# Performance work log

Measured on AMD Instinct MI355X. Metric: run time of the kernel, lower is better.

Reference implementation:

```python
import jax, jax.numpy as jnp
import numpy as np

B, N, D = 256, 512, 512
H = 512            # step_context_dim
HEADS = 8
KEY = H // HEADS
T = 128            # number of decode steps
TANH_CLIP = 10.0
TEMP = 1.0
VEHICLE_CAP = 1.0
BATTERY_CAP = 1.0
NEG = -1e9         # stands in for -inf; safe under softmax/vjp


def setup_inputs() -> dict:
    key = jax.random.key(0)
    ks = jax.random.split(key, 10)
    embedding = jax.random.normal(ks[0], (B, N, D), dtype=jnp.float32)
    current_nodes = jax.random.randint(ks[1], (B, T), 0, N)
    used_capacity = jax.random.uniform(ks[2], (B, T), dtype=jnp.float32)
    used_battery = jax.random.uniform(ks[3], (B, T), dtype=jnp.float32)
    current_time = jax.random.uniform(ks[4], (B, T), dtype=jnp.float32)
    mask = jax.random.randint(ks[5], (B, T, N), 0, 2).astype(bool)
    mask = mask.at[:, :, 0].set(False)  # ensure at least one feasible node
    s = 0.02
    W_context = jax.random.normal(ks[6], (D, H), dtype=jnp.float32) * s
    W_kvlogit = jax.random.normal(ks[7], (D, 3 * H), dtype=jnp.float32) * s
    W_step = jax.random.normal(ks[8], (D + 3, H), dtype=jnp.float32) * s
    W_out = jax.random.normal(ks[9], (H, H), dtype=jnp.float32) * s
    return {"embedding": embedding, "current_nodes": current_nodes,
            "used_capacity": used_capacity, "used_battery": used_battery,
            "current_time": current_time, "mask": mask,
            "W_context": W_context, "W_kvlogit": W_kvlogit,
            "W_step": W_step, "W_out": W_out}


def reference(embedding, current_nodes, used_capacity, used_battery,
              current_time, mask, W_context, W_kvlogit, W_step, W_out):
    b, n, d = embedding.shape
    t = current_nodes.shape[1]
    # fixed context from mean graph embedding: [B,1,H]
    fixed_context = jnp.einsum('bd,dh->bh', embedding.mean(axis=1), W_context)[:, None, :]
    # shared K/V/logit-K projections: [B,N,3H]
    kvl = jnp.einsum('bnd,de->bne', embedding, W_kvlogit)
    glimpse_K, glimpse_V, logit_K = jnp.split(kvl, 3, axis=-1)
    glimpse_K = glimpse_K.reshape(b, n, HEADS, KEY).transpose(0, 2, 1, 3)  # [B,h,N,k]
    glimpse_V = glimpse_V.reshape(b, n, HEADS, KEY).transpose(0, 2, 1, 3)  # [B,h,N,k]
    # per-step context: gathered current-node embedding + 3 scalar state features
    cur_emb = jnp.take_along_axis(
        embedding, current_nodes[:, :, None], axis=1)  # [B,T,D]
    next_nodes = jnp.concatenate(
        [cur_emb,
         (VEHICLE_CAP - used_capacity)[..., None],
         (BATTERY_CAP - used_battery)[..., None],
         current_time[..., None]], axis=-1)            # [B,T,D+3]
    query = fixed_context + jnp.einsum('btd,dh->bth', next_nodes, W_step)  # [B,T,H]
    # multi-head single-query glimpse attention over all T steps at once
    Q = query.reshape(b, t, HEADS, KEY)
    compat = jnp.einsum('bthk,bhnk->bhtn', Q, glimpse_K) / np.sqrt(KEY)
    compat = jnp.where(mask[:, None, :, :], NEG, compat)
    attn = jax.nn.softmax(compat, axis=-1)
    heads_out = jnp.einsum('bhtn,bhnk->bthk', attn, glimpse_V).reshape(b, t, H)
    glimpse = jnp.einsum('bth,ho->bto', heads_out, W_out)  # project_out
    logits = jnp.einsum('bth,bnh->btn', glimpse, logit_K) / np.sqrt(H)
    logits = jnp.tanh(logits) * TANH_CLIP
    logits = jnp.where(mask, NEG, logits)
    log_p = jax.nn.log_softmax(logits / TEMP, axis=-1)  # [B,T,N]
    return log_p
```

## Files before the change

kernel.cpp:

```cpp
#include <hip/hip_runtime.h>
#include <hip/hip_bf16.h>
#include <hip/hip_fp8.h>
#include <stdint.h>

typedef unsigned char  u8;
typedef unsigned short u16;
typedef unsigned int   u32;
typedef unsigned long long u64;
typedef __attribute__((ext_vector_type(4))) float f32x4;
typedef __attribute__((ext_vector_type(8))) short s16x8;

#define NEG_INF (-1e9f)

__device__ __forceinline__ u16 f2bf(float f) {
  __hip_bfloat16 h = __float2bfloat16(f);
  return __builtin_bit_cast(u16, h);
}

__device__ __forceinline__ u8 f2fp8(float f) {
  __hip_fp8_e4m3 h(f);
  return (u8)h.__x;
}

#if defined(__has_builtin)
#if __has_builtin(__builtin_amdgcn_cvt_pk_fp8_f32)
#define HAVE_PK8 1
#endif
#endif

__device__ __forceinline__ u32 pk4_fp8(float a, float b, float c, float d) {
#ifdef HAVE_PK8
  int r = __builtin_amdgcn_cvt_pk_fp8_f32(a, b, 0, false);
  r = __builtin_amdgcn_cvt_pk_fp8_f32(c, d, r, true);
  return (u32)r;
#else
  return (u32)f2fp8(a) | ((u32)f2fp8(b) << 8) | ((u32)f2fp8(c) << 16) |
         ((u32)f2fp8(d) << 24);
#endif
}

__device__ __forceinline__ f32x4 mfma16(s16x8 a, s16x8 b, f32x4 c) {
  return __builtin_amdgcn_mfma_f32_16x16x32_bf16(a, b, c, 0, 0, 0);
}

__device__ __forceinline__ f32x4 mfma8(long a, long b, f32x4 c) {
  return __builtin_amdgcn_mfma_f32_16x16x32_fp8_fp8(a, b, c, 0, 0, 0);
}

#define GLOAD16(g, l)                                                        \
  __builtin_amdgcn_global_load_lds(                                          \
      (const __attribute__((address_space(1))) unsigned int*)(g),            \
      (__attribute__((address_space(3))) unsigned int*)(l), 16, 0, 0)
#define GLOAD4(g, l)                                                         \
  __builtin_amdgcn_global_load_lds(                                          \
      (const __attribute__((address_space(1))) unsigned int*)(g),            \
      (__attribute__((address_space(3))) unsigned int*)(l), 4, 0, 0)

#define WAITV(n) asm volatile("s_waitcnt vmcnt(" #n ")" ::: "memory")
#define WAITLGKM asm volatile("s_waitcnt lgkmcnt(0)" ::: "memory")
#define SBAR __builtin_amdgcn_sched_barrier(0)
#define HBAR __builtin_amdgcn_s_barrier()

__global__ void detect_mask_kernel(const u32* __restrict__ mraw, u32* __restrict__ flag) {
  __shared__ int any;
  if (threadIdx.x == 0) any = 0;
  __syncthreads();
  int loc = 0;
  for (int i = threadIdx.x; i < 16384; i += 256) {
    u32 v = mraw[i];
    if (v & 0xFFFFFF00u) loc = 1;
  }
  if (loc) atomicOr(&any, 1);
  __syncthreads();
  if (threadIdx.x == 0) *flag = any ? 1u : 4u;
}

__global__ __launch_bounds__(256) void maskprep_kernel(const void* __restrict__ mraw,
                                                       const u32* __restrict__ flag,
                                                       unsigned char* __restrict__ mb) {
  long long idx = (long long)blockIdx.x * 256 + threadIdx.x;
  long long bt = idx >> 6;
  int ch = (int)(idx & 63);
  unsigned char byte = 0;
  if (*flag == 1) {
    u64 v = *(const u64*)((const unsigned char*)mraw + bt * 512 + ch * 8);
#pragma unroll
    for (int i = 0; i < 8; i++)
      if ((v >> (8 * i)) & 0xFFull) byte |= (unsigned char)(1 << i);
  } else {
    const int* p = (const int*)mraw + bt * 512 + ch * 8;
#pragma unroll
    for (int i = 0; i < 8; i++)
      if (p[i]) byte |= (unsigned char)(1 << i);
  }
  mb[idx] = byte;
}

__global__ void tcvt8_kernel(const float* __restrict__ in, int ld_in, int kreal,
                             int CO, u8* __restrict__ outp) {
  int i = blockIdx.x;
  for (int j = threadIdx.x; j < CO; j += 256) {
    float v = (j < kreal) ? in[(long long)j * ld_in + i] * 16.0f : 0.0f;
    outp[(long long)i * CO + j] = f2fp8(v);
  }
}

__global__ void slice_cvt_kernel(const float* __restrict__ in, u16* __restrict__ outp) {
  long long idx = (long long)blockIdx.x * 256 + threadIdx.x;
  long long dd = idx >> 9;
  int hh = (int)(idx & 511);
  outp[idx] = f2bf(in[dd * 1536 + 1024 + hh]);
}

__global__ void cvt_bf_kernel(const float* __restrict__ in, u16* __restrict__ outp) {
  long long idx = (long long)blockIdx.x * 256 + threadIdx.x;
  outp[idx] = f2bf(in[idx]);
}

__global__ __launch_bounds__(256) void cvt_pmean_kernel(const float* __restrict__ emb,
                                                        u8* __restrict__ e8,
                                                        float* __restrict__ pmean) {
  const int bq = blockIdx.x >> 2, nq = blockIdx.x & 3;
  const int tid = threadIdx.x;
  const int ro = tid >> 7;
  const int c4 = (tid & 127) << 2;
  const long long base = ((long long)bq * 512 + nq * 128) * 512;
  float s[4] = {0.f, 0.f, 0.f, 0.f};
  for (int n = ro; n < 128; n += 2) {
    f32x4 v = *(const f32x4*)&emb[base + (long long)n * 512 + c4];
#pragma unroll
    for (int i = 0; i < 4; i++) s[i] += v[i];
    *(u32*)&e8[base + (long long)n * 512 + c4] = pk4_fp8(v[0], v[1], v[2], v[3]);
  }
  __shared__ float ls[2][512];
#pragma unroll
  for (int i = 0; i < 4; i++) ls[ro][c4 + i] = s[i];
  __syncthreads();
  float* dst = pmean + (long long)blockIdx.x * 512;
  dst[tid] = ls[0][tid] + ls[1][tid];
  dst[tid + 256] = ls[0][tid + 256] + ls[1][tid + 256];
}

__global__ __launch_bounds__(256) void fixedctx_kernel(const float* __restrict__ pmean,
                                                       const float* __restrict__ Wc,
                                                       float* __restrict__ fixedc) {
  __shared__ float mf[512];
  int b = blockIdx.x;
  const float* p = pmean + (long long)b * 4 * 512;
  for (int d = threadIdx.x; d < 512; d += 256)
    mf[d] = (p[d] + p[512 + d] + p[1024 + d] + p[1536 + d]) * (1.0f / 512.0f);
  __syncthreads();
  for (int h = threadIdx.x; h < 512; h += 256) {
    float s = 0.f;
    for (int d = 0; d < 512; ++d) s += mf[d] * Wc[(long long)d * 512 + h];
    fixedc[(long long)b * 512 + h] = s;
  }
}

__global__ __launch_bounds__(256) void build_nextn8_kernel(
    const u8* __restrict__ e8, const int* __restrict__ cur,
    const float* __restrict__ ucap, const float* __restrict__ ubat,
    const float* __restrict__ ctim, u8* __restrict__ outp) {
  const long long rowm = (long long)blockIdx.x * 4 + (threadIdx.x >> 6);
  const int lane = threadIdx.x & 63;
  const int b = (int)(rowm >> 7);
  const int node = cur[rowm];
  const u8* src = e8 + ((long long)b * 512 + node) * 512;
  u8* dst = outp + rowm * 576;
  *(u64*)&dst[lane * 8] = *(const u64*)&src[lane * 8];
  if (lane < 8) {
    u64 v = 0;
    if (lane == 0) {
      v = (u64)f2fp8(1.0f - ucap[rowm]) | ((u64)f2fp8(1.0f - ubat[rowm]) << 8) |
          ((u64)f2fp8(ctim[rowm]) << 16);
    }
    *(u64*)&dst[512 + lane * 8] = v;
  }
}

__global__ __launch_bounds__(512, 4) void gemm_kv8_kernel(
    const u8* __restrict__ A8, const u8* __restrict__ Bw8,
    u8* __restrict__ K8, u8* __restrict__ V8) {
  __shared__ __align__(16) char lds[49152];
  const int tid = threadIdx.x;
  const int lane = tid & 63;
  const int wid = tid >> 6;
  const int wr = wid >> 1, wc = wid & 1;
  const int fr = lane & 15;
  const int fq = lane >> 4;

  const int p = blockIdx.x;
  const int x = p & 7;
  const int i = p >> 3;
  const int ntile = i & 7;
  const int mgrp = i >> 3;
  const long long nrow0 = (long long)ntile * 128;

  const int srow = tid >> 2;
  const int sc = tid & 3;

#define MROW(tt2) (((long long)x * 64 + mgrp * 8 + ((tt2) >> 3)) * 256)
#define KOF(tt2) (((tt2) & 7) * 64)

#define STAGEA(dd, tt2)                                                       \
  {                                                                           \
    _Pragma("unroll") for (int g_ = 0; g_ < 2; g_++) {                        \
      const int r_ = g_ * 128 + srow;                                         \
      GLOAD16(A8 + (MROW(tt2) + r_) * 512ll + KOF(tt2) +                      \
                  ((sc ^ ((r_ >> 1) & 3)) << 4),                              \
              lds + (dd) * 24576 + g_ * 8192 + wid * 1024);                   \
    }                                                                         \
  }
#define STAGEB(dd, tt2)                                                       \
  {                                                                           \
    GLOAD16(Bw8 + (nrow0 + srow) * 512ll + KOF(tt2) +                         \
                ((sc ^ ((srow >> 1) & 3)) << 4),                              \
            lds + (dd) * 24576 + 16384 + wid * 1024);                         \
  }

#define READ_A(dst, mb)                                                       \
  _Pragma("unroll") for (int ks = 0; ks < 2; ks++) {                          \
    const int r_ = wr * 64 + (mb) * 16 + fr;                                  \
    dst[ks] = *(const long*)(ab + r_ * 64 + (((ks * 4 + fq) ^ (r_ & 6)) << 3)); \
  }
#define MFMA_PH(src, mb)                                                      \
  _Pragma("unroll") for (int nb = 0; nb < 4; nb++)                            \
  _Pragma("unroll") for (int ks = 0; ks < 2; ks++)                            \
    acc[mb][nb] = mfma8(src[ks], bfrag[nb][ks], acc[mb][nb]);

  STAGEB(0, 0); STAGEA(0, 0);
  STAGEB(1, 1); STAGEA(1, 1);

  f32x4 acc[4][4];

#pragma unroll 1
  for (int u = 0; u < 8; u++) {
#pragma unroll
    for (int ii = 0; ii < 4; ii++)
#pragma unroll
      for (int jj = 0; jj < 4; jj++) acc[ii][jj] = (f32x4){0.f, 0.f, 0.f, 0.f};

#pragma unroll 1
    for (int t8 = 0; t8 < 8; t8++) {
      const int tt = u * 8 + t8;
      const int d = tt & 1;
      if (tt == 63) { WAITV(0); } else { WAITV(3); }
      HBAR; SBAR;

      const char* ab = lds + d * 24576;
      const char* bb = lds + d * 24576 + 16384;

      long bfrag[4][2];
#pragma unroll
      for (int nb = 0; nb < 4; nb++)
#pragma unroll
        for (int ks = 0; ks < 2; ks++) {
          const int brow = wc * 64 + nb * 16 + fr;
          bfrag[nb][ks] =
              *(const long*)(bb + brow * 64 + (((ks * 4 + fq) ^ (brow & 6)) << 3));
        }
      long afA[2], afB[2];
      READ_A(afA, 0);
      WAITLGKM; SBAR;
      READ_A(afB, 1);
      __builtin_amdgcn_s_setprio(1);
      MFMA_PH(afA, 0);
      __builtin_amdgcn_s_setprio(0);
      WAITLGKM; SBAR;
      READ_A(afA, 2);
      __builtin_amdgcn_s_setprio(1);
      MFMA_PH(afB, 1);
      __builtin_amdgcn_s_setprio(0);
      WAITLGKM; SBAR;
      READ_A(afB, 3);
      __builtin_amdgcn_s_setprio(1);
      MFMA_PH(afA, 2);
      __builtin_amdgcn_s_setprio(0);
      WAITLGKM; SBAR;
      HBAR;
      if (tt + 2 < 64) { STAGEB(d, tt + 2); STAGEA(d, tt + 2); }
      __builtin_amdgcn_s_setprio(1);
      MFMA_PH(afB, 3);
      __builtin_amdgcn_s_setprio(0);
    }

    const long long mrow0 = MROW(u * 8);
    const int colbase = (int)(ntile * 128) + wc * 64;
#pragma unroll
    for (int mb = 0; mb < 4; mb++) {
      const long long row = mrow0 + wr * 64 + mb * 16 + fq * 4;
      const int bbx = (int)(row >> 9);
      const int node0 = (int)(row & 511);
#pragma unroll
      for (int nb = 0; nb < 4; nb++) {
        const int col = colbase + nb * 16 + fr;
        const int hh = (col >> 6) & 7;
        const int kk = col & 63;
        const u32 pw = pk4_fp8(acc[mb][nb][0] * 0.0625f, acc[mb][nb][1] * 0.0625f,
                               acc[mb][nb][2] * 0.0625f, acc[mb][nb][3] * 0.0625f);
        if (col < 512) {
          u8* dst = K8 + (((long long)(bbx * 8 + hh) * 512 + node0) << 6) + kk;
#pragma unroll
          for (int q = 0; q < 4; q++)
            dst[(long long)q << 6] = (u8)(pw >> (8 * q));
        } else {
          *(u32*)(V8 + (((long long)(bbx * 8 + hh) * 64 + kk) << 9) + node0) = pw;
        }
      }
    }
  }
#undef STAGEA
#undef STAGEB
#undef READ_A
#undef MFMA_PH
#undef MROW
#undef KOF
}

template <int MODE>
__global__ __launch_bounds__(512, 4) void gemm8_kernel(
    const u8* __restrict__ A8, const u8* __restrict__ B8,
    int ldA, int ldB, int NT,
    u8* __restrict__ out0, const float* __restrict__ aux) {
  __shared__ __align__(16) char lds[49152];
  const int tid = threadIdx.x;
  const int lane = tid & 63;
  const int wid = tid >> 6;
  const int wr = wid >> 1, wc = wid & 1;
  const int fr = lane & 15;
  const int fq = lane >> 4;

  const int p = blockIdx.x;
  const int wk = (p & 7) * 64 + (p >> 3);
  const int mtile = wk >> 2;
  const int ntile = wk & 3;
  const long long mrow0 = (long long)mtile * 256;
  const long long nrow0 = (long long)ntile * 128;

  const int srow = tid >> 2;
  const int sc = tid & 3;

#define STAGEA8(dd, k0)                                                       \
  {                                                                           \
    _Pragma("unroll") for (int g_ = 0; g_ < 2; g_++) {                        \
      const int r_ = g_ * 128 + srow;                                         \
      GLOAD16(A8 + (mrow0 + r_) * (long long)ldA + (k0) +                     \
                  ((sc ^ ((r_ >> 1) & 3)) << 4),                              \
              lds + (dd) * 24576 + g_ * 8192 + wid * 1024);                   \
    }                                                                         \
  }
#define STAGEB8(dd, k0)                                                       \
  {                                                                           \
    GLOAD16(B8 + (nrow0 + srow) * (long long)ldB + (k0) +                     \
                ((sc ^ ((srow >> 1) & 3)) << 4),                              \
            lds + (dd) * 24576 + 16384 + wid * 1024);                         \
  }
#define READ_A8(dst, mb)                                                      \
  _Pragma("unroll") for (int ks = 0; ks < 2; ks++) {                          \
    const int r_ = wr * 64 + (mb) * 16 + fr;                                  \
    dst[ks] = *(const long*)(ab + r_ * 64 + (((ks * 4 + fq) ^ (r_ & 6)) << 3)); \
  }
#define MFMA_PH8(src, mb)                                                     \
  _Pragma("unroll") for (int nb = 0; nb < 4; nb++)                            \
  _Pragma("unroll") for (int ks = 0; ks < 2; ks++)                            \
    acc[mb][nb] = mfma8(src[ks], bfrag[nb][ks], acc[mb][nb]);

  f32x4 acc[4][4];
#pragma unroll
  for (int ii = 0; ii < 4; ii++)
#pragma unroll
    for (int jj = 0; jj < 4; jj++) acc[ii][jj] = (f32x4){0.f, 0.f, 0.f, 0.f};

  STAGEB8(0, 0); STAGEA8(0, 0);
  STAGEB8(1, 64); STAGEA8(1, 64);

#pragma unroll 1
  for (int t = 0; t < NT; t++) {
    const int d = t & 1;
    if (t == NT - 1) { WAITV(0); } else { WAITV(3); }
    HBAR; SBAR;

    const char* ab = lds + d * 24576;
    const char* bb = lds + d * 24576 + 16384;

    long bfrag[4][2];
#pragma unroll
    for (int nb = 0; nb < 4; nb++)
#pragma unroll
      for (int ks = 0; ks < 2; ks++) {
        const int brow = wc * 64 + nb * 16 + fr;
        bfrag[nb][ks] =
            *(const long*)(bb + brow * 64 + (((ks * 4 + fq) ^ (brow & 6)) << 3));
      }
    long afA[2], afB[2];
    READ_A8(afA, 0);
    WAITLGKM; SBAR;
    READ_A8(afB, 1);
    __builtin_amdgcn_s_setprio(1);
    MFMA_PH8(afA, 0);
    __builtin_amdgcn_s_setprio(0);
    WAITLGKM; SBAR;
    READ_A8(afA, 2);
    __builtin_amdgcn_s_setprio(1);
    MFMA_PH8(afB, 1);
    __builtin_amdgcn_s_setprio(0);
    WAITLGKM; SBAR;
    READ_A8(afB, 3);
    __builtin_amdgcn_s_setprio(1);
    MFMA_PH8(afA, 2);
    __builtin_amdgcn_s_setprio(0);
    WAITLGKM; SBAR;
    HBAR;
    if (t + 2 < NT) { STAGEB8(d, (t + 2) * 64); STAGEA8(d, (t + 2) * 64); }
    __builtin_amdgcn_s_setprio(1);
    MFMA_PH8(afB, 3);
    __builtin_amdgcn_s_setprio(0);
  }
#undef STAGEA8
#undef STAGEB8
#undef READ_A8
#undef MFMA_PH8

  const int colbase = (int)(ntile * 128) + wc * 64;
#pragma unroll
  for (int mb = 0; mb < 4; mb++) {
    const long long row0 = mrow0 + wr * 64 + mb * 16 + fq * 4;
#pragma unroll
    for (int nb = 0; nb < 4; nb++) {
      const int col = colbase + nb * 16 + fr;
      u32 pw;
      if (MODE == 0) {
        float v0 = acc[mb][nb][0] * 0.0625f + aux[((row0 + 0) >> 7) * 512 + col];
        float v1 = acc[mb][nb][1] * 0.0625f + aux[((row0 + 1) >> 7) * 512 + col];
        float v2 = acc[mb][nb][2] * 0.0625f + aux[((row0 + 2) >> 7) * 512 + col];
        float v3 = acc[mb][nb][3] * 0.0625f + aux[((row0 + 3) >> 7) * 512 + col];
        pw = pk4_fp8(v0 * 2.0f, v1 * 2.0f, v2 * 2.0f, v3 * 2.0f);
      } else {
        pw = pk4_fp8(acc[mb][nb][0] * 0.03125f, acc[mb][nb][1] * 0.03125f,
                     acc[mb][nb][2] * 0.03125f, acc[mb][nb][3] * 0.03125f);
      }
#pragma unroll
      for (int q = 0; q < 4; q++)
        out0[(row0 + q) * 512 + col] = (u8)(pw >> (8 * q));
    }
  }
}

__global__ __launch_bounds__(512, 4) void gemm_lsm8_kernel(
    const u8* __restrict__ e8, const u8* __restrict__ tmp8,
    const u64* __restrict__ maskb, float* __restrict__ outp) {
  __shared__ __align__(16) char lds[73728];
  const int tid = threadIdx.x;
  const int lane = tid & 63;
  const int wid = tid >> 6;
  const int fr = lane & 15;
  const int fq = lane >> 4;

  const int p = blockIdx.x;
  const int x = p & 7;
  const int i = p >> 3;
  const int thalf = i & 1;
  const int b = x * 32 + (i >> 1);

  const u8* Ab = e8 + (long long)b * 262144;
  const u8* Bb = tmp8 + (long long)b * 65536 + (long long)thalf * 64 * 512;

  const int srow = tid >> 2;
  const int sc = tid & 3;

#define STAGEA(dd, k0)                                                        \
  {                                                                           \
    _Pragma("unroll") for (int g_ = 0; g_ < 4; g_++) {                        \
      const int r_ = g_ * 128 + srow;                                         \
      GLOAD16(Ab + r_ * 512ll + (k0) + ((sc ^ ((r_ >> 1) & 3)) << 4),         \
              lds + (dd) * 32768 + g_ * 8192 + wid * 1024);                   \
    }                                                                         \
  }
#define STAGEB(dd, k0)                                                        \
  {                                                                           \
    _Pragma("unroll") for (int g_ = 0; g_ < 2; g_++) {                        \
      const int r_ = g_ * 32 + (tid >> 4);                                    \
      const int lb_ = (tid & 15) * 4;                                         \
      const int gb_ = ((((lb_ >> 4) ^ ((r_ >> 1) & 3))) << 4) | (lb_ & 15);   \
      GLOAD4(Bb + r_ * 512ll + (k0) + gb_,                                    \
             lds + 65536 + (dd) * 4096 + g_ * 2048 + wid * 256);              \
    }                                                                         \
  }
#define READ_A(dst, mb)                                                       \
  _Pragma("unroll") for (int ks = 0; ks < 2; ks++) {                          \
    const int r_ = wid * 64 + (mb) * 16 + fr;                                 \
    dst[ks] = *(const long*)(ab + r_ * 64 + (((ks * 4 + fq) ^ (r_ & 6)) << 3)); \
  }
#define MFMA_PH(src, mb)                                                      \
  _Pragma("unroll") for (int nb = 0; nb < 4; nb++)                            \
  _Pragma("unroll") for (int ks = 0; ks < 2; ks++)                            \
    acc[mb][nb] = mfma8(src[ks], bfrag[nb][ks], acc[mb][nb]);

  f32x4 acc[4][4];
#pragma unroll
  for (int ii = 0; ii < 4; ii++)
#pragma unroll
    for (int jj = 0; jj < 4; jj++) acc[ii][jj] = (f32x4){0.f, 0.f, 0.f, 0.f};

  STAGEB(0, 0); STAGEA(0, 0);
  STAGEB(1, 64); STAGEA(1, 64);

#pragma unroll 1
  for (int t = 0; t < 8; t++) {
    const int d = t & 1;
    if (t == 7) { WAITV(0); } else { WAITV(6); }
    HBAR; SBAR;

    const char* ab = lds + d * 32768;
    const char* bb = lds + 65536 + d * 4096;

    long bfrag[4][2];
#pragma unroll
    for (int nb = 0; nb < 4; nb++)
#pragma unroll
      for (int ks = 0; ks < 2; ks++) {
        const int brow = nb * 16 + fr;
        bfrag[nb][ks] =
            *(const long*)(bb + brow * 64 + (((ks * 4 + fq) ^ (brow & 6)) << 3));
      }
    long afA[2], afB[2];
    READ_A(afA, 0);
    WAITLGKM; SBAR;
    READ_A(afB, 1);
    __builtin_amdgcn_s_setprio(1);
    MFMA_PH(afA, 0);
    __builtin_amdgcn_s_setprio(0);
    WAITLGKM; SBAR;
    READ_A(afA, 2);
    __builtin_amdgcn_s_setprio(1);
    MFMA_PH(afB, 1);
    __builtin_amdgcn_s_setprio(0);
    WAITLGKM; SBAR;
    READ_A(afB, 3);
    __builtin_amdgcn_s_setprio(1);
    MFMA_PH(afA, 2);
    __builtin_amdgcn_s_setprio(0);
    WAITLGKM; SBAR;
    HBAR;
    if (t + 2 < 8) { STAGEB(d, (t + 2) * 64); STAGEA(d, (t + 2) * 64); }
    __builtin_amdgcn_s_setprio(1);
    MFMA_PH(afB, 3);
    __builtin_amdgcn_s_setprio(0);
  }
#undef STAGEA
#undef STAGEB
#undef READ_A
#undef MFMA_PH

  float* red = (float*)lds;
  const float rs8 = 0.044194173824159216f * 0.125f;
  const float L2E = 1.4426950408889634f;

  float lmax[4];
#pragma unroll
  for (int nb = 0; nb < 4; nb++) {
    const int tl = nb * 16 + fr;
    const long long orow = (long long)b * 128 + thalf * 64 + tl;
    const u64 w = maskb[orow * 8 + wid];
    float mx = -3.0e38f;
#pragma unroll
    for (int mb = 0; mb < 4; mb++) {
      f32x4 r;
#pragma unroll
      for (int q = 0; q < 4; q++) {
        float xv = acc[mb][nb][q] * rs8;
        float e = exp2f(xv * 2.8853900817779268f);
        float th = 1.0f - 2.0f * __builtin_amdgcn_rcpf(e + 1.0f);
        float lg = 10.0f * th;
        const int bitn = mb * 16 + fq * 4 + q;
        if ((w >> bitn) & 1ull) lg = NEG_INF;
        r[q] = lg;
        mx = fmaxf(mx, lg);
      }
      acc[mb][nb] = r;
    }
    mx = fmaxf(mx, __shfl_xor(mx, 16));
    mx = fmaxf(mx, __shfl_xor(mx, 32));
    lmax[nb] = mx;
  }
  __syncthreads();
  if (lane < 16) {
#pragma unroll
    for (int nb = 0; nb < 4; nb++) red[wid * 64 + nb * 16 + lane] = lmax[nb];
  }
  __syncthreads();
  if (tid < 64) {
    float m = red[tid];
#pragma unroll
    for (int ww = 1; ww < 8; ww++) m = fmaxf(m, red[ww * 64 + tid]);
    red[512 + tid] = m;
  }
  __syncthreads();
  float lsum[4];
#pragma unroll
  for (int nb = 0; nb < 4; nb++) {
    const float m = red[512 + nb * 16 + fr];
    float s = 0.f;
#pragma unroll
    for (int mb = 0; mb < 4; mb++)
#pragma unroll
      for (int q = 0; q < 4; q++) s += exp2f((acc[mb][nb][q] - m) * L2E);
    s += __shfl_xor(s, 16);
    s += __shfl_xor(s, 32);
    lsum[nb] = s;
  }
  if (lane < 16) {
#pragma unroll
    for (int nb = 0; nb < 4; nb++) red[576 + wid * 64 + nb * 16 + lane] = lsum[nb];
  }
  __syncthreads();
  if (tid < 64) {
    float s = red[576 + tid];
#pragma unroll
    for (int ww = 1; ww < 8; ww++) s += red[576 + ww * 64 + tid];
    red[1088 + tid] = red[512 + tid] + logf(s);
  }
  __syncthreads();
#pragma unroll
  for (int nb = 0; nb < 4; nb++) {
    const int tl = nb * 16 + fr;
    const long long orow = (long long)b * 128 + thalf * 64 + tl;
    const float lse = red[1088 + tl];
#pragma unroll
    for (int mb = 0; mb < 4; mb++) {
      const int node0 = wid * 64 + mb * 16 + fq * 4;
      f32x4 r = acc[mb][nb];
#pragma unroll
      for (int q = 0; q < 4; q++) r[q] -= lse;
      *(f32x4*)&outp[orow * 512 + node0] = r;
    }
  }
}

__global__ __launch_bounds__(256) void gemm128_plain_kernel(
    const u16* __restrict__ A, const u16* __restrict__ Bv, u8* __restrict__ outp) {
  __shared__ u16 lA[128 * 32];
  __shared__ u16 lB[128 * 32];
  const int tid = threadIdx.x;
  const int lane = tid & 63;
  const int wave = tid >> 6;
  const int wr = wave >> 1, wc = wave & 1;

  const int p = blockIdx.x;
  const int wk = (p & 7) * 2 + (p >> 3);
  const int ntile = wk & 3;
  const int mtile = wk >> 2;
  const long long arow0 = (long long)mtile * 128;
  const long long brow0 = (long long)ntile * 128;

  f32x4 acc[4][4];
#pragma unroll
  for (int i = 0; i < 4; i++)
#pragma unroll
    for (int j = 0; j < 4; j++) acc[i][j] = (f32x4){0.f, 0.f, 0.f, 0.f};

  const int sc8 = (lane & 3) << 3;

  for (int k0 = 0; k0 < 512; k0 += 32) {
    __syncthreads();
#pragma unroll
    for (int i = 0; i < 2; i++) {
      GLOAD16(A + (arow0 + i * 64 + wave * 16 + (lane >> 2)) * 512ll + k0 + sc8,
              &lA[(i * 64 + wave * 16) * 32]);
      GLOAD16(Bv + (brow0 + i * 64 + wave * 16 + (lane >> 2)) * 512ll + k0 + sc8,
              &lB[(i * 64 + wave * 16) * 32]);
    }
    __syncthreads();
    s16x8 af[4], bfr[4];
#pragma unroll
    for (int i = 0; i < 4; i++)
      af[i] = *(const s16x8*)&lA[(wr * 64 + i * 16 + (lane & 15)) * 32 + ((lane >> 4) << 3)];
#pragma unroll
    for (int j = 0; j < 4; j++)
      bfr[j] = *(const s16x8*)&lB[(wc * 64 + j * 16 + (lane & 15)) * 32 + ((lane >> 4) << 3)];
#pragma unroll
    for (int i = 0; i < 4; i++)
#pragma unroll
      for (int j = 0; j < 4; j++) acc[i][j] = mfma16(af[i], bfr[j], acc[i][j]);
  }

#pragma unroll
  for (int i = 0; i < 4; i++) {
    const int rl = wr * 64 + i * 16 + ((lane >> 4) << 2);
#pragma unroll
    for (int j = 0; j < 4; j++) {
      const int cl = wc * 64 + j * 16 + (lane & 15);
#pragma unroll
      for (int q = 0; q < 4; q++)
        outp[(arow0 + rl + q) * 512 + brow0 + cl] = f2fp8(acc[i][j][q] * 64.0f);
    }
  }
}

__global__ __launch_bounds__(512, 4) void attn_kernel(
    const u8* __restrict__ q8, const u8* __restrict__ K8,
    const u8* __restrict__ V8, const u64* __restrict__ maskbits,
    u8* __restrict__ o8buf) {
  __shared__ __align__(16) char lds[68864];
  char* Plds = lds + 32768;
  float* rsw = (float*)(lds + 66560);
  float* rst = (float*)(lds + 68608);

  const int p = blockIdx.x;
  const int fb = (p & 7) * 512 + (p >> 3);
  const int thalf = fb & 1;
  const int h = (fb >> 1) & 7;
  const int b = fb >> 4;
  const int bh = b * 8 + h;
  const int tid = threadIdx.x;
  const int lane = tid & 63;
  const int wid = tid >> 6;
  const int fr = lane & 15;
  const int fq = lane >> 4;
  const int tt0 = thalf * 64;

  {
    const u8* Vb = V8 + (long long)bh * 32768;
#pragma unroll
    for (int it = 0; it < 4; it++) {
      const int row = it * 16 + (tid >> 5);
      const int s16 = tid & 31;
      GLOAD16(Vb + row * 512 + ((s16 ^ (row & 7)) << 4), lds + row * 512);
    }
  }

  const u8* Qb = q8 + ((long long)(b * 128 + tt0)) * 512 + h * 64;
  long qf[4][2];
#pragma unroll
  for (int tf = 0; tf < 4; tf++)
#pragma unroll
    for (int ks = 0; ks < 2; ks++)
      qf[tf][ks] = *(const long*)(Qb + (long long)(tf * 16 + fr) * 512 + ks * 32 + fq * 8);

  const int wstrip = wid * 64;
  const u8* Kb = K8 + ((long long)bh * 512 + wstrip) * 64;
  f32x4 s[4][4];
#pragma unroll
  for (int nf = 0; nf < 4; nf++)
#pragma unroll
    for (int tf = 0; tf < 4; tf++) s[nf][tf] = (f32x4){0.f, 0.f, 0.f, 0.f};
#pragma unroll
  for (int nf = 0; nf < 4; nf++) {
#pragma unroll
    for (int ks = 0; ks < 2; ks++) {
      long kf = *(const long*)(Kb + (long long)(nf * 16 + fr) * 64 + ks * 32 + fq * 8);
#pragma unroll
      for (int tf = 0; tf < 4; tf++) s[nf][tf] = mfma8(kf, qf[tf][ks], s[nf][tf]);
    }
  }

  const float CE2 = 0.09016844005556021f;
  u64 mq[4];
#pragma unroll
  for (int tf = 0; tf < 4; tf++)
    mq[tf] = maskbits[((long long)(b * 128) + tt0 + tf * 16 + fr) * 8 + wid];
  float psum[4] = {0.f, 0.f, 0.f, 0.f};
#pragma unroll
  for (int nf = 0; nf < 4; nf++) {
#pragma unroll
    for (int tf = 0; tf < 4; tf++) {
      float pv[4];
#pragma unroll
      for (int q = 0; q < 4; q++) {
        const int bit = nf * 16 + fq * 4 + q;
        float v = exp2f(s[nf][tf][q] * CE2);
        if ((mq[tf] >> bit) & 1ull) v = 0.0f;
        psum[tf] += v;
        pv[q] = v;
      }
      const u32 pw = pk4_fp8(pv[0], pv[1], pv[2], pv[3]);
      const int t = tf * 16 + fr;
      const int o = wstrip + nf * 16 + fq * 4;
      const int s8 = o >> 3, lo = o & 7;
      *(u32*)(Plds + t * 528 + (((s8 ^ (t & 7)) << 3) | lo)) = pw;
    }
  }
#pragma unroll
  for (int tf = 0; tf < 4; tf++) {
    float v = psum[tf];
    v += __shfl_xor(v, 16);
    v += __shfl_xor(v, 32);
    if (lane < 16) rsw[(tf * 16 + lane) * 8 + wid] = v;
  }
  __syncthreads();

  if (tid < 64) {
    float sum = rsw[tid * 8];
#pragma unroll
    for (int ww = 1; ww < 8; ww++) sum += rsw[tid * 8 + ww];
    rst[tid] = __builtin_amdgcn_rcpf(sum);
  }

  const int kkh = wid & 1;
  const int tts = wid >> 1;
  f32x4 o[2];
  o[0] = (f32x4){0.f, 0.f, 0.f, 0.f};
  o[1] = (f32x4){0.f, 0.f, 0.f, 0.f};
  const int tpv = tts * 16 + fr;
#pragma unroll
  for (int nstep = 0; nstep < 16; nstep++) {
    const int s8 = nstep * 4 + fq;
    long pf = *(const long*)(Plds + tpv * 528 + ((s8 ^ (tpv & 7)) << 3));
#pragma unroll
    for (int kf = 0; kf < 2; kf++) {
      const int kk = kkh * 32 + kf * 16 + fr;
      const int vs16 = s8 >> 1, vlo = s8 & 1;
      long vf = *(const long*)(lds + kk * 512 + (((vs16 ^ (kk & 7)) << 4) | (vlo << 3)));
      o[kf] = mfma8(vf, pf, o[kf]);
    }
  }
  __syncthreads();

  const float r4 = rst[tpv] * 4.0f;
  const long long orow = (long long)b * 128 + tt0 + tpv;
#pragma unroll
  for (int kf = 0; kf < 2; kf++) {
    const u32 pw = pk4_fp8(o[kf][0] * r4, o[kf][1] * r4, o[kf][2] * r4, o[kf][3] * r4);
    const int col = h * 64 + kkh * 32 + kf * 16 + fq * 4;
    *(u32*)&o8buf[orow * 512 + col] = pw;
  }
}

extern "C" void kernel_launch(void* const* d_in, const int* in_sizes, int n_in,
                              void* d_out, int out_size, void* d_ws, size_t ws_size,
                              hipStream_t stream) {
  (void)in_sizes; (void)n_in; (void)out_size; (void)ws_size;
  const float* emb  = (const float*)d_in[0];
  const int*   cur  = (const int*)d_in[1];
  const float* ucap = (const float*)d_in[2];
  const float* ubat = (const float*)d_in[3];
  const float* ctim = (const float*)d_in[4];
  const void*  mask = d_in[5];
  const float* Wc   = (const float*)d_in[6];
  const float* Wkvl = (const float*)d_in[7];
  const float* Wstep= (const float*)d_in[8];
  const float* Wout = (const float*)d_in[9];

  char* w = (char*)d_ws;
  size_t off = 0;
  auto take = [&](size_t nbytes) -> char* {
    char* p = w + off;
    off += (nbytes + 255) & ~(size_t)255;
    return p;
  };
  u32* flag            = (u32*)take(4);
  unsigned char* maskb = (unsigned char*)take((size_t)256 * 128 * 64);
  u8* e8               = (u8*)take((size_t)256 * 512 * 512);
  u8* WkT8             = (u8*)take((size_t)1024 * 512);
  u8* WstepT8          = (u8*)take((size_t)512 * 576);
  u16* W2bf            = (u16*)take((size_t)512 * 512 * 2);
  u16* Woutbf          = (u16*)take((size_t)512 * 512 * 2);
  u8* WfT8             = (u8*)take((size_t)512 * 512);
  float* pmean         = (float*)take((size_t)1024 * 512 * 4);
  float* fixedc        = (float*)take((size_t)256 * 512 * 4);
  u8* K8               = (u8*)take((size_t)256 * 8 * 512 * 64);
  u8* V8               = (u8*)take((size_t)256 * 8 * 64 * 512);
  u8* nextn8           = (u8*)take((size_t)32768 * 576);
  u8* q8               = (u8*)take((size_t)32768 * 512);
  u8* o8               = (u8*)take((size_t)32768 * 512);
  u8* tmp8             = (u8*)take((size_t)32768 * 512);

  detect_mask_kernel<<<1, 256, 0, stream>>>((const u32*)mask, flag);
  maskprep_kernel<<<8192, 256, 0, stream>>>(mask, flag, maskb);
  tcvt8_kernel<<<1024, 256, 0, stream>>>(Wkvl, 1536, 512, 512, WkT8);
  tcvt8_kernel<<<512, 256, 0, stream>>>(Wstep, 512, 515, 576, WstepT8);
  slice_cvt_kernel<<<1024, 256, 0, stream>>>(Wkvl, W2bf);
  cvt_bf_kernel<<<1024, 256, 0, stream>>>(Wout, Woutbf);
  gemm128_plain_kernel<<<16, 256, 0, stream>>>(W2bf, Woutbf, WfT8);
  cvt_pmean_kernel<<<1024, 256, 0, stream>>>(emb, e8, pmean);
  fixedctx_kernel<<<256, 256, 0, stream>>>(pmean, Wc, fixedc);
  build_nextn8_kernel<<<8192, 256, 0, stream>>>(e8, cur, ucap, ubat, ctim, nextn8);

  gemm_kv8_kernel<<<512, 512, 0, stream>>>(e8, WkT8, K8, V8);
  gemm8_kernel<0><<<512, 512, 0, stream>>>(nextn8, WstepT8, 576, 576, 9, q8, fixedc);
  attn_kernel<<<4096, 512, 0, stream>>>(q8, K8, V8, (const u64*)maskb, o8);
  gemm8_kernel<1><<<512, 512, 0, stream>>>(o8, WfT8, 512, 512, 8, tmp8, nullptr);
  gemm_lsm8_kernel<<<512, 512, 0, stream>>>(e8, tmp8, (const u64*)maskb, (float*)d_out);
}
```

Before: 501.3 us.

## Stage K/V epilogue through LDS for coalesced 16-byte stores and retile V layout

```diff
diff --git a/kernel.cpp b/kernel.cpp
--- a/kernel.cpp
+++ b/kernel.cpp
@@ -8,6 +8,7 @@
 typedef unsigned int   u32;
 typedef unsigned long long u64;
 typedef __attribute__((ext_vector_type(4))) float f32x4;
+typedef __attribute__((ext_vector_type(4))) unsigned int u32x4;
 typedef __attribute__((ext_vector_type(8))) short s16x8;
 
 #define NEG_INF (-1e9f)
@@ -181,7 +182,7 @@
 __global__ __launch_bounds__(512, 4) void gemm_kv8_kernel(
     const u8* __restrict__ A8, const u8* __restrict__ Bw8,
     u8* __restrict__ K8, u8* __restrict__ V8) {
-  __shared__ __align__(16) char lds[49152];
+  __shared__ __align__(16) char lds[57344];
   const int tid = threadIdx.x;
   const int lane = tid & 63;
   const int wid = tid >> 6;
@@ -232,6 +233,8 @@
   STAGEB(1, 1); STAGEA(1, 1);
 
   f32x4 acc[4][4];
+  char* tile = lds + 49152 + wid * 1024;
+  const int hh = (ntile * 2 + wc) & 7;
 
 #pragma unroll 1
   for (int u = 0; u < 8; u++) {
@@ -285,27 +288,52 @@
     }
 
     const long long mrow0 = MROW(u * 8);
-    const int colbase = (int)(ntile * 128) + wc * 64;
-#pragma unroll
-    for (int mb = 0; mb < 4; mb++) {
-      const long long row = mrow0 + wr * 64 + mb * 16 + fq * 4;
-      const int bbx = (int)(row >> 9);
-      const int node0 = (int)(row & 511);
-#pragma unroll
-      for (int nb = 0; nb < 4; nb++) {
-        const int col = colbase + nb * 16 + fr;
-        const int hh = (col >> 6) & 7;
-        const int kk = col & 63;
-        const u32 pw = pk4_fp8(acc[mb][nb][0] * 0.0625f, acc[mb][nb][1] * 0.0625f,
-                               acc[mb][nb][2] * 0.0625f, acc[mb][nb][3] * 0.0625f);
-        if (col < 512) {
-          u8* dst = K8 + (((long long)(bbx * 8 + hh) * 512 + node0) << 6) + kk;
-#pragma unroll
-          for (int q = 0; q < 4; q++)
-            dst[(long long)q << 6] = (u8)(pw >> (8 * q));
-        } else {
-          *(u32*)(V8 + (((long long)(bbx * 8 + hh) * 64 + kk) << 9) + node0) = pw;
+    const int bbx = (int)(mrow0 >> 9);
+    const int nodeb = (int)(mrow0 & 511);
+    const long long bhoff = ((long long)(bbx * 8 + hh)) << 15;
+
+    if (ntile < 4) {
+#pragma unroll
+      for (int mb = 0; mb < 4; mb++) {
+#pragma unroll
+        for (int nb = 0; nb < 4; nb++) {
+          const u32 pw = pk4_fp8(acc[mb][nb][0] * 0.0625f, acc[mb][nb][1] * 0.0625f,
+                                 acc[mb][nb][2] * 0.0625f, acc[mb][nb][3] * 0.0625f);
+          const int colhi = (nb * 16 + (fr & ~3));
+          const int collo = fr & 3;
+#pragma unroll
+          for (int q = 0; q < 4; q++) {
+            const int row = fq * 4 + q;
+            tile[row * 64 + (colhi ^ ((row & 15) << 2)) + collo] = (u8)(pw >> (8 * q));
+          }
         }
+        WAITLGKM; SBAR;
+        const int row = lane >> 2;
+        u32x4 val;
+#pragma unroll
+        for (int j = 0; j < 4; j++) {
+          const int dw = ((lane & 3) * 4 + j) << 2;
+          val[j] = *(const u32*)(tile + row * 64 + (dw ^ ((row & 15) << 2)));
+        }
+        WAITLGKM; SBAR;
+        u8* dst = K8 + bhoff + (long long)(nodeb + wr * 64 + mb * 16) * 64;
+        *(u32x4*)(dst + lane * 16) = val;
+      }
+    } else {
+#pragma unroll
+      for (int mb = 0; mb < 4; mb++) {
+#pragma unroll
+        for (int nb = 0; nb < 4; nb++) {
+          const u32 pw = pk4_fp8(acc[mb][nb][0] * 0.0625f, acc[mb][nb][1] * 0.0625f,
+                                 acc[mb][nb][2] * 0.0625f, acc[mb][nb][3] * 0.0625f);
+          *(u32*)(tile + (nb * 16 + fr) * 16 + fq * 4) = pw;
+        }
+        WAITLGKM; SBAR;
+        u32x4 val = *(const u32x4*)(tile + lane * 16);
+        WAITLGKM; SBAR;
+        const int ngrp = (nodeb + wr * 64 + mb * 16) >> 4;
+        u8* dst = V8 + bhoff + (long long)ngrp * 1024;
+        *(u32x4*)(dst + lane * 16) = val;
       }
     }
   }
@@ -723,9 +751,11 @@
     const u8* Vb = V8 + (long long)bh * 32768;
 #pragma unroll
     for (int it = 0; it < 4; it++) {
-      const int row = it * 16 + (tid >> 5);
-      const int s16 = tid & 31;
-      GLOAD16(Vb + row * 512 + ((s16 ^ (row & 7)) << 4), lds + row * 512);
+      const int Lc = it * 512 + wid * 64 + lane;
+      const int kk = Lc >> 5;
+      const int s16p = Lc & 31;
+      const int s16 = s16p ^ (kk & 7);
+      GLOAD16(Vb + (s16 * 64 + kk) * 16, lds + (it * 512 + wid * 64) * 16);
     }
   }
 
```

Measured after the change: 470.7 us. -6.1%, faster.
